# Kernel optimization log

Hardware: AMD Instinct MI355X
Metric: run time of the kernel (lower is better)

The kernel has to match this reference:

```python
import jax, jax.numpy as jnp
import numpy as np
from jax import lax

ANGRES = 5


def _conv(x, w, stride=(1, 1), pad=((1, 1), (1, 1)), dil=(1, 1)):
    return lax.conv_general_dilated(x, w, stride, pad, rhs_dilation=dil,
                                    dimension_numbers=('NCHW', 'OIHW', 'NCHW'))


def _lrelu(x):
    return jnp.where(x >= 0, x, 0.1 * x)


def _block_s(x, w):
    # SAI input: split into 5x5 grid of (sh,sw) views, conv each view, emit MacPI-interleaved layout
    B, C, H, W = x.shape
    sh, sw = H // 5, W // 5
    p = x.reshape(B, C, 5, sh, 5, sw).transpose(0, 2, 4, 1, 3, 5).reshape(B * 25, C, sh, sw)
    y = _conv(p, w).reshape(B, 5, 5, C, sh, sw)
    # (B,bi,bj,C,sh,sw) -> (B,C,sh,bi,sw,bj) -> (B,C,H,W)   [torch permute(0,3,4,1,5,2)]
    return y.transpose(0, 3, 4, 1, 5, 2).reshape(B, C, H, W)


def _block_a(x, w):
    # MacPI input: conv each 5x5 macropixel independently (zero pad at block edges)
    B, C, H, W = x.shape
    nh, nw = H // 5, W // 5
    p = x.reshape(B, C, nh, 5, nw, 5).transpose(0, 2, 4, 1, 3, 5).reshape(B * nh * nw, C, 5, 5)
    y = _conv(p, w)
    return y.reshape(B, nh, nw, C, 5, 5).transpose(0, 3, 1, 4, 2, 5).reshape(B, C, H, W)


def _epi(x, w1, w2, a):
    # EPI conv: [1,3a] kernel, stride [1,a], pad [0,a]; then 1x1 to a*C; then 1D pixel shuffle on W
    y = _lrelu(_conv(x, w1, stride=(1, a), pad=((0, 0), (a, a))))
    y = _lrelu(_conv(y, w2, pad=((0, 0), (0, 0))))
    B, aC, H, Wa = y.shape
    C = aC // a
    return y.reshape(B, a, C, H, Wa).transpose(0, 2, 3, 4, 1).reshape(B, C, H, Wa * a)


def _att_fuse(buf, alpha, gamma, beta, eps=1e-5):
    # covariance-based GLU attention over the N=4 branches
    B, NC, H, W = buf.shape
    N = 4
    C = NC // N
    x5 = buf.reshape(B, N, C, H, W)
    xr = x5.reshape(B, N, C * H * W)
    M = xr.shape[-1]
    xc = xr - jnp.mean(xr, axis=-1, keepdims=True)
    cov = jnp.einsum('bnm,bkm->bnk', xc, xc) * (alpha / (M - 1))  # [B,N,N]
    norm = cov / jnp.sqrt(jnp.mean(cov * cov, axis=(1, 2), keepdims=True) + eps)
    g = gamma * norm + beta
    att = g * jax.nn.sigmoid(g)  # GLU of duplicated halves
    out = jnp.einsum('bnk,bkm->bnm', att, xr).reshape(B, N, C, H, W) + x5
    return out.reshape(B, NC, H, W)


def _mac2sai(x, a):
    B, C, HU, WV = x.shape
    h, w = HU // a, WV // a
    return x.reshape(B, C, a, h, a, w).transpose(0, 1, 3, 5, 2, 4).reshape(B, C, h * a, w * a)


def _tsfefb(x, x1, ws, wa, we1, we2, al, ga, be, wf1, wf2, a):
    feaSpa = _lrelu(_block_s(x1, ws))
    feaAng = _lrelu(_block_a(x, wa))
    feaH = _epi(x, we1, we2, a)
    feaV = jnp.transpose(_epi(jnp.transpose(x, (0, 1, 3, 2)), we1, we2, a), (0, 1, 3, 2))
    buf = jnp.concatenate([feaSpa, feaAng, feaH, feaV], axis=1)
    out = _att_fuse(buf, al, ga, be)
    y = _lrelu(_conv(out, wf1, pad=((0, 0), (0, 0))))
    y = _conv(y, wf2, pad=((a, a), (a, a)), dil=(a, a))
    return y + x


def setup_inputs() -> dict:
    key = jax.random.key(0)
    ks = jax.random.split(key, 12)
    B, C, a, n = 4, 64, ANGRES, 4
    H = W = a * 32  # 160

    def w(k, shape):
        fan_in = float(np.prod(shape[2:]))
        return jax.random.normal(k, shape, jnp.float32) / np.float32(np.sqrt(fan_in))

    return {
        'x': jax.random.normal(ks[0], (B, C, H, W), jnp.float32),
        'x1': jax.random.normal(ks[1], (B, C, H, W), jnp.float32),
        'w_spa': w(ks[2], (n, C, C, 3, 3)),
        'w_ang': w(ks[3], (n, C, C, 3, 3)),
        'w_epi1': w(ks[4], (n, C, C, 1, 3 * a)),
        'w_epi2': w(ks[5], (n, a * C, C, 1, 1)),
        'alpha': jnp.ones((n,), jnp.float32),
        'gamma': 0.1 * jax.random.normal(ks[6], (n,), jnp.float32),
        'beta': 0.1 * jax.random.normal(ks[7], (n,), jnp.float32),
        'w_fuse1': w(ks[8], (n, C, 4 * C, 1, 1)),
        'w_fuse2': w(ks[9], (n, C, C, 3, 3)),
    }


def reference(x, x1, w_spa, w_ang, w_epi1, w_epi2, alpha, gamma, beta, w_fuse1, w_fuse2):
    a = ANGRES
    buf, buf1 = x, x1
    for i in range(w_spa.shape[0]):
        buf = _tsfefb(buf, buf1, w_spa[i], w_ang[i], w_epi1[i], w_epi2[i],
                      alpha[i], gamma[i], beta[i], w_fuse1[i], w_fuse2[i], a)
        buf1 = _mac2sai(buf, a)
    return buf
```

## Files before the change

### kernel.cpp

```cpp
#include <hip/hip_runtime.h>

__device__ __forceinline__ float lrelu(float v){ return v >= 0.f ? v : 0.1f*v; }


__global__ __launch_bounds__(256) void k_wrep(const float* __restrict__ wspa, const float* __restrict__ wang,
                                              const float* __restrict__ wf2, float* __restrict__ outp){
  int id = blockIdx.x*256 + threadIdx.x;
  int t = id / 147456, r = id - t*147456;
  int i = r / 36864,  e = r - i*36864;
  int ci = e / 576,   r3 = e - ci*576;
  int co = r3 / 9,    j = r3 - co*9;
  const float* src = (t==0 ? wspa : (t==1 ? wang : wf2));
  outp[id] = src[(size_t)i*36864 + co*576 + ci*9 + j];
}

__global__ __launch_bounds__(256) void k_spa(const float* __restrict__ buf1, const float* __restrict__ w,
                                             float* __restrict__ out){
  const int P = blockIdx.x;
  const int within = P >> 3, cog = within & 7, tsel = within >> 3;
  const int tg = (P & 7)*25 + tsel;
  const int b = tg / 50, r2 = tg % 50;
  const int view = r2 >> 1, half = r2 & 1;
  const int bi = view / 5, bj = view % 5;
  const int th0 = half*16;
  const int tid = threadIdx.x;
  __shared__ float plane[2][18*38];
  for (int idx=tid; idx<2*18*38; idx+=256) ((float*)plane)[idx]=0.f;
  float acc[2][8];
  #pragma unroll
  for (int k=0;k<2;k++)
    #pragma unroll
    for (int c=0;c<8;c++) acc[k][c]=0.f;
  const float* src = buf1 + (size_t)b*1638400 + bi*32*160 + bj*32;
  const int sr = tid >> 3, sq = (tid & 7)*4;
  const int vr = th0 - 1 + sr;
  const bool rowok = (tid < 144) && ((unsigned)vr < 32u);
  __syncthreads();
  if (rowok)
    *(float4*)&plane[0][sr*38 + 4 + sq] = *(const float4*)(src + vr*160 + sq);
  __syncthreads();
  const int lr2 = tid >> 5, c = tid & 31;
  for (int ci=0; ci<64; ci++){
    float4 nx;
    const bool ld = rowok && (ci < 63);
    if (ld) nx = *(const float4*)(src + (size_t)(ci+1)*25600 + vr*160 + sq);
    const float* P2 = plane[ci & 1];
    float g[4][3];
    {
      const float* pp = &P2[(2*lr2)*38 + c + 3];
      g[0][0]=pp[0];   g[0][1]=pp[1];   g[0][2]=pp[2];
      g[1][0]=pp[38];  g[1][1]=pp[39];  g[1][2]=pp[40];
      g[2][0]=pp[76];  g[2][1]=pp[77];  g[2][2]=pp[78];
      g[3][0]=pp[114]; g[3][1]=pp[115]; g[3][2]=pp[116];
    }
    const float* wrow = w + ci*576 + cog*72;
    #pragma unroll
    for (int co=0;co<8;co++){
      const float* wp = wrow + co*9;
      float w0=wp[0],w1=wp[1],w2=wp[2],w3=wp[3],w4=wp[4],w5=wp[5],w6=wp[6],w7=wp[7],w8=wp[8];
      acc[0][co] += g[0][0]*w0+g[0][1]*w1+g[0][2]*w2+g[1][0]*w3+g[1][1]*w4
                  + g[1][2]*w5+g[2][0]*w6+g[2][1]*w7+g[2][2]*w8;
      acc[1][co] += g[1][0]*w0+g[1][1]*w1+g[1][2]*w2+g[2][0]*w3+g[2][1]*w4
                  + g[2][2]*w5+g[3][0]*w6+g[3][1]*w7+g[3][2]*w8;
    }
    if (ld) *(float4*)&plane[(ci+1)&1][sr*38 + 4 + sq] = nx;
    __syncthreads();
  }
  #pragma unroll
  for (int k=0;k<2;k++){
    int si = th0 + 2*lr2 + k;
    int h = si*5 + bi, wq = c*5 + bj;
    #pragma unroll
    for (int co=0;co<8;co++){
      int ch = b*64 + cog*8 + co;
      out[(size_t)ch*25600 + h*160 + wq] = lrelu(acc[k][co]);
    }
  }
}

__global__ __launch_bounds__(320) void k_ang(const float* __restrict__ bufA, const float* __restrict__ w,
                                             float* __restrict__ out){
  const int P = blockIdx.x;
  const int within = P >> 3, cog = within & 15, tsel = within >> 4;
  const int tg = (P & 7)*8 + tsel;
  const int b = tg >> 4, mip = tg & 15;
  const int tid = threadIdx.x;
  __shared__ float lds[2][2296];
  for (int i=tid; i<2*2296; i+=320) ((float*)lds)[i] = 0.f;

  const int u = tid >> 6, mi_l = (tid >> 5) & 1, mp = tid & 31;
  int ro[3];
  #pragma unroll
  for (int du=0; du<3; du++)
    ro[du] = mi_l*1148 + (u+du)*164 + mp*5;
  const bool st1 = tid < 80;
  const int rr0 = tid/40,       q0 = tid%40;
  const int rr1 = (tid+320)/40, q1 = (tid+320)%40;
  const int dst0 = (rr0/5)*1148 + (1 + rr0%5)*164 + q0*4;
  const int dst1 = (rr1/5)*1148 + (1 + rr1%5)*164 + q1*4;
  const float* src = bufA + (size_t)b*1638400 + (size_t)(mip*10)*160;

  float acc[4][5];
  #pragma unroll
  for (int co=0;co<4;co++)
    #pragma unroll
    for (int v=0;v<5;v++) acc[co][v]=0.f;

  __syncthreads();
  {
    *(float4*)&lds[0][dst0] = *(const float4*)(src + rr0*160 + q0*4);
    if (st1)
      *(float4*)&lds[0][dst1] = *(const float4*)(src + rr1*160 + q1*4);
  }
  __syncthreads();
  for (int ci=0; ci<64; ci++){
    float4 n0, n1;
    if (ci < 63){
      n0 = *(const float4*)(src + (size_t)(ci+1)*25600 + rr0*160 + q0*4);
      if (st1) n1 = *(const float4*)(src + (size_t)(ci+1)*25600 + rr1*160 + q1*4);
    }
    const float* Pb = lds[ci & 1];
    float c[3][5];
    #pragma unroll
    for (int du=0;du<3;du++){
      const float* rp = &Pb[ro[du]];
      c[du][0]=rp[0]; c[du][1]=rp[1]; c[du][2]=rp[2]; c[du][3]=rp[3]; c[du][4]=rp[4];
    }
    const float* wrow = w + ci*576 + cog*36;
    #pragma unroll
    for (int co=0;co<4;co++){
      const float* wp = wrow + co*9;
      float w0=wp[0],w1=wp[1],w2=wp[2],w3=wp[3],w4=wp[4],w5=wp[5],w6=wp[6],w7=wp[7],w8=wp[8];
      acc[co][0] += c[0][0]*w1 + c[0][1]*w2
                  + c[1][0]*w4 + c[1][1]*w5
                  + c[2][0]*w7 + c[2][1]*w8;
      acc[co][1] += c[0][0]*w0 + c[0][1]*w1 + c[0][2]*w2
                  + c[1][0]*w3 + c[1][1]*w4 + c[1][2]*w5
                  + c[2][0]*w6 + c[2][1]*w7 + c[2][2]*w8;
      acc[co][2] += c[0][1]*w0 + c[0][2]*w1 + c[0][3]*w2
                  + c[1][1]*w3 + c[1][2]*w4 + c[1][3]*w5
                  + c[2][1]*w6 + c[2][2]*w7 + c[2][3]*w8;
      acc[co][3] += c[0][2]*w0 + c[0][3]*w1 + c[0][4]*w2
                  + c[1][2]*w3 + c[1][3]*w4 + c[1][4]*w5
                  + c[2][2]*w6 + c[2][3]*w7 + c[2][4]*w8;
      acc[co][4] += c[0][3]*w0 + c[0][4]*w1
                  + c[1][3]*w3 + c[1][4]*w4
                  + c[2][3]*w6 + c[2][4]*w7;
    }
    if (ci < 63){
      float* Q = lds[(ci+1)&1];
      *(float4*)&Q[dst0] = n0;
      if (st1) *(float4*)&Q[dst1] = n1;
    }
    __syncthreads();
  }
  const int h = (mip*2 + mi_l)*5 + u;
  const int wc0 = mp*5;
  #pragma unroll
  for (int co=0;co<4;co++){
    int ch = b*64 + cog*4 + co;
    float* op = out + (size_t)ch*25600 + (size_t)h*160 + wc0;
    op[0]=lrelu(acc[co][0]); op[1]=lrelu(acc[co][1]); op[2]=lrelu(acc[co][2]);
    op[3]=lrelu(acc[co][3]); op[4]=lrelu(acc[co][4]);
  }
}

__global__ __launch_bounds__(320) void k_epi(const float* __restrict__ bufA, const float* __restrict__ we1,
                                             const float* __restrict__ we2, float* __restrict__ out){
  const int bb = blockIdx.x >> 1, half = blockIdx.x & 1;
  const int b = bb / 160, hw = bb % 160;
  const int tid = threadIdx.x;
  __shared__ float rowp[64*96];
  __shared__ float y1s[64*16];
  const int lofs = half ? 0 : 8;
  const int xofs = half ? 72 : 0;
  for (int ft=tid; ft<1408; ft+=320){
    int ci = ft/22, q = ft - ci*22;
    *(float4*)&rowp[ci*96 + lofs + q*4] =
      *(const float4*)(bufA + (size_t)b*1638400 + (size_t)ci*25600 + (size_t)hw*160 + xofs + q*4);
  }
  for (int idx=tid; idx<512; idx+=320){
    int ci = idx>>3, j = idx&7;
    rowp[ci*96 + (half ? 88+j : j)] = 0.f;
  }
  __syncthreads();
  if (tid < 256){
    const int co = tid >> 2, wvl0 = (tid & 3)*4;
    const int a0 = 2 + wvl0*5;
    float acc[4];
    #pragma unroll
    for (int j=0;j<4;j++) acc[j]=0.f;
    const float* wp0 = we1 + (size_t)co*960;
    for (int ci=0; ci<64; ci++){
      float fl[32];
      const float* rp = &rowp[ci*96 + a0];
      #pragma unroll
      for (int m=0;m<16;m++) *(float2*)&fl[2*m] = *(const float2*)&rp[2*m];
      const float* wp = wp0 + ci*15;
      #pragma unroll
      for (int t=0;t<15;t++){
        float wt = wp[t];
        #pragma unroll
        for (int j=0;j<4;j++) acc[j] += fl[1 + j*5 + t]*wt;
      }
    }
    #pragma unroll
    for (int j=0;j<4;j++) y1s[co*16 + wvl0 + j] = lrelu(acc[j]);
  }
  __syncthreads();
  {
    const int oc = tid, kk = oc >> 6, c = oc & 63;
    float a2[16];
    #pragma unroll
    for (int wv=0;wv<16;wv++) a2[wv]=0.f;
    const float* wp = we2 + (size_t)oc*64;
    for (int ci=0; ci<64; ci++){
      float wt = wp[ci];
      const float* yp = &y1s[ci*16];
      #pragma unroll
      for (int wv=0; wv<16; wv++) a2[wv] += yp[wv]*wt;
    }
    float* y2s = rowp;
    #pragma unroll
    for (int wv=0; wv<16; wv++) y2s[c*84 + wv*5 + kk] = lrelu(a2[wv]);
  }
  __syncthreads();
  {
    const float* y2s = rowp;
    for (int k=0;k<4;k++){
      int f = (tid + k*320)*4;
      int c = f/80, rr = f - c*80;
      *(float4*)(out + (size_t)(b*64+c)*25600 + (size_t)hw*160 + half*80 + rr)
        = *(const float4*)&y2s[c*84+rr];
    }
  }
}

__global__ __launch_bounds__(256) void k_permV(const float* __restrict__ tmp, float* __restrict__ dst){
  const int bc = blockIdx.x;
  const int ti = blockIdx.y / 5, tj = blockIdx.y % 5;
  const int hw0 = ti*32, r0 = tj*32;
  const int lx = threadIdx.x & 31, ly = threadIdx.x >> 5;
  __shared__ float tile[32][33];
  const float* in = tmp + (size_t)bc*25600;
  float* outp = dst + (size_t)bc*25600;
  for (int yy=ly; yy<32; yy+=8)
    tile[yy][lx] = in[(size_t)(hw0+yy)*160 + r0 + lx];
  __syncthreads();
  for (int yy=ly; yy<32; yy+=8)
    outp[(size_t)(r0+yy)*160 + hw0 + lx] = tile[lx][yy];
}

__global__ __launch_bounds__(256) void k_permM(const float* __restrict__ A, float* __restrict__ dst){
  const int bc = blockIdx.x >> 5, hh = blockIdx.x & 31;
  const int tid = threadIdx.x;
  __shared__ float rows[5*160];
  const float* in = A + (size_t)bc*25600;
  if (tid < 200){
    int ai = tid/40, q = (tid - ai*40)*4;
    *(float4*)&rows[ai*160 + q] = *(const float4*)(in + (size_t)(ai*32+hh)*160 + q);
  }
  __syncthreads();
  float* outp = dst + (size_t)bc*25600 + (size_t)hh*800;
  for (int t=tid; t<800; t+=256){
    int ww = t/25, r2 = t - ww*25, ai = r2/5, aj = r2 - ai*5;
    outp[t] = rows[ai*160 + aj*32 + ww];
  }
}

__global__ __launch_bounds__(256) void k_red(const float* __restrict__ b0, const float* __restrict__ b1,
                                             const float* __restrict__ b2, const float* __restrict__ b3,
                                             float* __restrict__ part){
  const int b = blockIdx.y, blk = blockIdx.x;
  const int tid = threadIdx.x;
  const size_t off = (size_t)b*1638400 + (size_t)blk*25600;
  float s0=0,s1=0,s2=0,s3=0;
  float p00=0,p01=0,p02=0,p03=0,p11=0,p12=0,p13=0,p22=0,p23=0,p33=0;
  for (int it=0; it<25; it++){
    size_t m = off + it*1024 + tid*4;
    float4 x0 = *(const float4*)(b0+m);
    float4 x1 = *(const float4*)(b1+m);
    float4 x2 = *(const float4*)(b2+m);
    float4 x3 = *(const float4*)(b3+m);
    s0 += (x0.x+x0.y)+(x0.z+x0.w);
    s1 += (x1.x+x1.y)+(x1.z+x1.w);
    s2 += (x2.x+x2.y)+(x2.z+x2.w);
    s3 += (x3.x+x3.y)+(x3.z+x3.w);
    p00 += x0.x*x0.x+x0.y*x0.y+x0.z*x0.z+x0.w*x0.w;
    p01 += x0.x*x1.x+x0.y*x1.y+x0.z*x1.z+x0.w*x1.w;
    p02 += x0.x*x2.x+x0.y*x2.y+x0.z*x2.z+x0.w*x2.w;
    p03 += x0.x*x3.x+x0.y*x3.y+x0.z*x3.z+x0.w*x3.w;
    p11 += x1.x*x1.x+x1.y*x1.y+x1.z*x1.z+x1.w*x1.w;
    p12 += x1.x*x2.x+x1.y*x2.y+x1.z*x2.z+x1.w*x2.w;
    p13 += x1.x*x3.x+x1.y*x3.y+x1.z*x3.z+x1.w*x3.w;
    p22 += x2.x*x2.x+x2.y*x2.y+x2.z*x2.z+x2.w*x2.w;
    p23 += x2.x*x3.x+x2.y*x3.y+x2.z*x3.z+x2.w*x3.w;
    p33 += x3.x*x3.x+x3.y*x3.y+x3.z*x3.z+x3.w*x3.w;
  }
  float vals[14] = {s0,s1,s2,s3,p00,p01,p02,p03,p11,p12,p13,p22,p23,p33};
  __shared__ float red[4][14];
  int lane = tid & 63, wv = tid >> 6;
  #pragma unroll
  for (int j=0;j<14;j++){
    float v = vals[j];
    #pragma unroll
    for (int o=32;o>0;o>>=1) v += __shfl_down(v,o,64);
    if (lane==0) red[wv][j]=v;
  }
  __syncthreads();
  if (tid<14) part[((size_t)b*64+blk)*16 + tid] = red[0][tid]+red[1][tid]+red[2][tid]+red[3][tid];
}

__global__ __launch_bounds__(256) void k_attW(const float* __restrict__ part,
        const float* __restrict__ alpha, const float* __restrict__ gamma, const float* __restrict__ beta,
        int iblk, const float* __restrict__ wf1, float* __restrict__ Weff){
  const int b = blockIdx.x, tid = threadIdx.x;
  __shared__ float st[14];
  __shared__ float att[16];
  if (tid<14){
    float t=0;
    for (int blk=0;blk<64;blk++) t += part[((size_t)b*64+blk)*16 + tid];
    st[tid]=t;
  }
  __syncthreads();
  if (tid==0){
    const float M = 1638400.f;
    float s[4] = {st[0],st[1],st[2],st[3]};
    float S[4][4];
    S[0][0]=st[4];  S[0][1]=S[1][0]=st[5];  S[0][2]=S[2][0]=st[6];  S[0][3]=S[3][0]=st[7];
    S[1][1]=st[8];  S[1][2]=S[2][1]=st[9];  S[1][3]=S[3][1]=st[10];
    S[2][2]=st[11]; S[2][3]=S[3][2]=st[12]; S[3][3]=st[13];
    float al=alpha[iblk], ga=gamma[iblk], be=beta[iblk];
    float scale = al/(M-1.f);
    float cov[4][4], ss=0.f;
    for (int n=0;n<4;n++) for (int k=0;k<4;k++){
      float c = (S[n][k] - s[n]*s[k]/M)*scale;
      cov[n][k]=c; ss += c*c;
    }
    float rms = sqrtf(ss/16.f + 1e-5f);
    for (int n=0;n<4;n++) for (int k=0;k<4;k++){
      float g = ga*cov[n][k]/rms + be;
      att[n*4+k] = g/(1.f+expf(-g));
    }
  }
  __syncthreads();
  for (int idx=tid; idx<16384; idx+=256){
    int co=idx>>8, kc=idx&255, k=kc>>6, c=kc&63;
    float v = wf1[co*256+kc];
    #pragma unroll
    for (int n=0;n<4;n++) v += att[n*4+k]*wf1[co*256+n*64+c];
    Weff[(size_t)b*16384+idx] = v;
  }
}

__global__ __launch_bounds__(256) void k_fuse1(const float* b0, const float* __restrict__ b1,
                                               const float* __restrict__ b2, const float* __restrict__ b3,
                                               const float* __restrict__ Weff, float* y64){
  const int tile = blockIdx.x, b = blockIdx.y;
  const int px0 = tile*64;
  const int tid = threadIdx.x;
  const int ti = tid >> 4, tj = tid & 15;
  __shared__ float xs[64][68];
  __shared__ float wt[64][68];
  float acc[4][4];
  #pragma unroll
  for (int i=0;i<4;i++)
    #pragma unroll
    for (int j=0;j<4;j++) acc[i][j]=0.f;
  const float* bptr[4] = {b0,b1,b2,b3};
  for (int kb=0; kb<4; kb++){
    const float* xbk = bptr[kb] + (size_t)b*1638400 + px0;
    const float* wb = Weff + (size_t)b*16384 + kb*64;
    __syncthreads();
    for (int idx=tid; idx<4096; idx+=256){
      int kc=idx>>6, px=idx&63;
      xs[kc][px] = xbk[(size_t)kc*25600 + px];
    }
    for (int idx=tid; idx<4096; idx+=256){
      int co=idx>>6, k2=idx&63;
      wt[k2][co] = wb[co*256 + k2];
    }
    __syncthreads();
    for (int k2=0;k2<64;k2++){
      float4 a = *(const float4*)&wt[k2][ti*4];
      float4 v = *(const float4*)&xs[k2][tj*4];
      acc[0][0]+=a.x*v.x; acc[0][1]+=a.x*v.y; acc[0][2]+=a.x*v.z; acc[0][3]+=a.x*v.w;
      acc[1][0]+=a.y*v.x; acc[1][1]+=a.y*v.y; acc[1][2]+=a.y*v.z; acc[1][3]+=a.y*v.w;
      acc[2][0]+=a.z*v.x; acc[2][1]+=a.z*v.y; acc[2][2]+=a.z*v.z; acc[2][3]+=a.z*v.w;
      acc[3][0]+=a.w*v.x; acc[3][1]+=a.w*v.y; acc[3][2]+=a.w*v.z; acc[3][3]+=a.w*v.w;
    }
  }
  #pragma unroll
  for (int i=0;i<4;i++){
    int co = ti*4 + i;
    float4 o = make_float4(lrelu(acc[i][0]), lrelu(acc[i][1]), lrelu(acc[i][2]), lrelu(acc[i][3]));
    *(float4*)(y64 + ((size_t)(b*64+co))*25600 + px0 + tj*4) = o;
  }
}

template<int FINAL>
__global__ __launch_bounds__(256) void k_fuse2(const float* __restrict__ y64, const float* resid,
                                               const float* __restrict__ w, float* outp){
  const int P = blockIdx.x;
  const int within = P >> 3, cog = within & 7, tsel = within >> 3;
  const int tg = (P & 7)*25 + tsel;
  const int b = tg / 50, tile = tg % 50;
  const int th0 = (tile/5)*16, tw0 = (tile%5)*32;
  const int tid = threadIdx.x;
  __shared__ float plane[2][26*48];
  float acc[2][8];
  #pragma unroll
  for (int k=0;k<2;k++)
    #pragma unroll
    for (int c=0;c<8;c++) acc[k][c]=0.f;
  const float* src = y64 + (size_t)b*1638400;
  const int s0r = tid/12,        s0c = tid - (tid/12)*12;
  const int s1i = tid + 256;
  const int s1r = s1i/12,        s1c = s1i - (s1i/12)*12;
  const bool has1 = tid < 56;
  const int g0h = th0 - 5 + s0r, g0w = tw0 - 8 + s0c*4;
  const int g1h = th0 - 5 + s1r, g1w = tw0 - 8 + s1c*4;
  const bool v0 = ((unsigned)g0h < 160u) && ((unsigned)g0w < 160u);
  const bool v1 = has1 && ((unsigned)g1h < 160u) && ((unsigned)g1w < 160u);
  const int go0 = g0h*160 + g0w, go1 = g1h*160 + g1w;
  const int d0 = s0r*48 + s0c*4, d1 = s1r*48 + s1c*4;
  const float4 z4 = make_float4(0.f,0.f,0.f,0.f);
  {
    float4 x0 = v0 ? *(const float4*)(src + go0) : z4;
    *(float4*)&plane[0][d0] = x0;
    if (has1){
      float4 x1 = v1 ? *(const float4*)(src + go1) : z4;
      *(float4*)&plane[0][d1] = x1;
    }
  }
  __syncthreads();
  const int lr = tid >> 5, c = tid & 31;
  const int tap = lr*48 + c + 3;
  for (int ci=0; ci<64; ci++){
    float4 n0, n1;
    if (ci < 63){
      const float* sN = src + (size_t)(ci+1)*25600;
      n0 = v0 ? *(const float4*)(sN + go0) : z4;
      if (has1) n1 = v1 ? *(const float4*)(sN + go1) : z4;
    }
    const float* Pb = plane[ci & 1];
    float t0[9], t1[9];
    {
      const float* pp = &Pb[tap];
      t0[0]=pp[0];      t0[1]=pp[5];      t0[2]=pp[10];
      t0[3]=pp[240];    t0[4]=pp[245];    t0[5]=pp[250];
      t0[6]=pp[480];    t0[7]=pp[485];    t0[8]=pp[490];
      const float* qq = pp + 8*48;
      t1[0]=qq[0];      t1[1]=qq[5];      t1[2]=qq[10];
      t1[3]=qq[240];    t1[4]=qq[245];    t1[5]=qq[250];
      t1[6]=qq[480];    t1[7]=qq[485];    t1[8]=qq[490];
    }
    const float* wrow = w + ci*576 + cog*72;
    #pragma unroll
    for (int co=0;co<8;co++){
      const float* wp = wrow + co*9;
      float w0=wp[0],w1=wp[1],w2=wp[2],w3=wp[3],w4=wp[4],w5=wp[5],w6=wp[6],w7=wp[7],w8=wp[8];
      acc[0][co] += t0[0]*w0+t0[1]*w1+t0[2]*w2+t0[3]*w3+t0[4]*w4
                  + t0[5]*w5+t0[6]*w6+t0[7]*w7+t0[8]*w8;
      acc[1][co] += t1[0]*w0+t1[1]*w1+t1[2]*w2+t1[3]*w3+t1[4]*w4
                  + t1[5]*w5+t1[6]*w6+t1[7]*w7+t1[8]*w8;
    }
    if (ci < 63){
      float* Q = plane[(ci+1)&1];
      *(float4*)&Q[d0] = n0;
      if (has1) *(float4*)&Q[d1] = n1;
    }
    __syncthreads();
  }
  #pragma unroll
  for (int k=0;k<2;k++){
    int h = th0 + lr + k*8, wq = tw0 + c;
    #pragma unroll
    for (int co=0;co<8;co++){
      int cg = cog*8 + co;
      size_t base = ((size_t)(b*64+cg)*160 + h)*160 + wq;
      outp[base] = acc[k][co] + resid[base];
    }
  }
}

extern "C" void kernel_launch(void* const* d_in, const int* in_sizes, int n_in,
                              void* d_out, int out_size, void* d_ws, size_t ws_size,
                              hipStream_t stream){
  const float* x    = (const float*)d_in[0];
  const float* x1   = (const float*)d_in[1];
  const float* wspa = (const float*)d_in[2];
  const float* wang = (const float*)d_in[3];
  const float* we1  = (const float*)d_in[4];
  const float* we2  = (const float*)d_in[5];
  const float* al   = (const float*)d_in[6];
  const float* ga   = (const float*)d_in[7];
  const float* be   = (const float*)d_in[8];
  const float* wf1  = (const float*)d_in[9];
  const float* wf2  = (const float*)d_in[10];

  char* ws = (char*)d_ws;
  const size_t SLOT = 26214400;
  float* A  = (float*)(ws);
  float* Bv = (float*)(ws +   SLOT);
  float* T1 = (float*)(ws + 2*SLOT);
  float* T2 = (float*)(ws + 3*SLOT);
  float* part = (float*)(ws + 4*SLOT);
  float* Weff = (float*)(ws + 4*SLOT + 16384);
  float* Wrep = (float*)(ws + 4*SLOT + 16384 + 262144);
  float* WspaR = Wrep;
  float* WangR = Wrep + 147456;
  float* Wf2R  = Wrep + 2*147456;
  float* D = (float*)d_out;

  k_wrep<<<1728,256,0,stream>>>(wspa, wang, wf2, Wrep);

  for (int i=0;i<4;i++){
    const float* Asrc  = (i==0) ? x  : (const float*)A;
    const float* B1src = (i==0) ? x1 : (const float*)Bv;
    k_permV<<<dim3(256,25),256,0,stream>>>(Asrc, D);
    k_epi<<<1280,320,0,stream>>>(D, we1 + (size_t)i*61440, we2 + (size_t)i*20480, T2);
    k_spa<<<1600,256,0,stream>>>(B1src, WspaR + (size_t)i*36864, T1);
    k_permV<<<dim3(256,25),256,0,stream>>>(T2, Bv);
    k_ang<<<1024,320,0,stream>>>(Asrc, WangR + (size_t)i*36864, T2);
    k_epi<<<1280,320,0,stream>>>(Asrc, we1 + (size_t)i*61440, we2 + (size_t)i*20480, D);
    k_red<<<dim3(64,4),256,0,stream>>>(T1, T2, D, Bv, part);
    k_attW<<<4,256,0,stream>>>(part, al, ga, be, i, wf1 + (size_t)i*16384, Weff);
    k_fuse1<<<dim3(400,4),256,0,stream>>>(T1, T2, D, Bv, Weff, T1);
    if (i<3){
      k_fuse2<0><<<1600,256,0,stream>>>(T1, Asrc, Wf2R + (size_t)i*36864, A);
      k_permM<<<8192,256,0,stream>>>(A, Bv);
    } else {
      k_fuse2<1><<<1600,256,0,stream>>>(T1, Asrc, Wf2R + (size_t)i*36864, D);
    }
  }
}
```

Measured before the change: 2.807 ms.

## Give each wavefront a private LDS halo tile to drop block-wide barriers in spa and fuse2 convs

In the spatial 3x3 conv and the fuse2 dilated conv, each 64-lane wavefront now stages its own haloed input rows in a private double-buffered LDS region instead of sharing one block-wide plane. This removes the __syncthreads at every input-channel step and relies on wavefront-lockstep execution for LDS visibility. The cost is redundant halo loads across wavefronts (more global and LDS traffic) and a larger shared footprint. Correctness depends on implicit wave-level ordering, with no explicit wave barrier.

```diff
diff --git a/kernel.cpp b/kernel.cpp
--- a/kernel.cpp
+++ b/kernel.cpp
@@ -24,34 +24,34 @@
   const int bi = view / 5, bj = view % 5;
   const int th0 = half*16;
   const int tid = threadIdx.x;
-  __shared__ float plane[2][18*38];
-  for (int idx=tid; idx<2*18*38; idx+=256) ((float*)plane)[idx]=0.f;
+  const int wv = tid >> 6, lane = tid & 63;
+  __shared__ float wl[4][2][240];
+  for (int i=lane; i<480; i+=64) ((float*)wl[wv])[i] = 0.f;
   float acc[2][8];
   #pragma unroll
   for (int k=0;k<2;k++)
     #pragma unroll
-    for (int c=0;c<8;c++) acc[k][c]=0.f;
+    for (int c2=0;c2<8;c2++) acc[k][c2]=0.f;
   const float* src = buf1 + (size_t)b*1638400 + bi*32*160 + bj*32;
-  const int sr = tid >> 3, sq = (tid & 7)*4;
-  const int vr = th0 - 1 + sr;
-  const bool rowok = (tid < 144) && ((unsigned)vr < 32u);
-  __syncthreads();
+  const int srow = lane >> 3, sq = (lane & 7)*4;
+  const int vr = th0 + 4*wv - 1 + srow;
+  const bool rowok = (lane < 48) && ((unsigned)vr < 32u);
+  const int dst = srow*40 + 4 + sq;
   if (rowok)
-    *(float4*)&plane[0][sr*38 + 4 + sq] = *(const float4*)(src + vr*160 + sq);
-  __syncthreads();
-  const int lr2 = tid >> 5, c = tid & 31;
+    *(float4*)&wl[wv][0][dst] = *(const float4*)(src + vr*160 + sq);
+  const int lrl = (tid >> 5) & 1, c = tid & 31;
   for (int ci=0; ci<64; ci++){
     float4 nx;
     const bool ld = rowok && (ci < 63);
     if (ld) nx = *(const float4*)(src + (size_t)(ci+1)*25600 + vr*160 + sq);
-    const float* P2 = plane[ci & 1];
+    const float* Pb = wl[wv][ci & 1];
     float g[4][3];
     {
-      const float* pp = &P2[(2*lr2)*38 + c + 3];
+      const float* pp = &Pb[(2*lrl)*40 + c + 3];
       g[0][0]=pp[0];   g[0][1]=pp[1];   g[0][2]=pp[2];
-      g[1][0]=pp[38];  g[1][1]=pp[39];  g[1][2]=pp[40];
-      g[2][0]=pp[76];  g[2][1]=pp[77];  g[2][2]=pp[78];
-      g[3][0]=pp[114]; g[3][1]=pp[115]; g[3][2]=pp[116];
+      g[1][0]=pp[40];  g[1][1]=pp[41];  g[1][2]=pp[42];
+      g[2][0]=pp[80];  g[2][1]=pp[81];  g[2][2]=pp[82];
+      g[3][0]=pp[120]; g[3][1]=pp[121]; g[3][2]=pp[122];
     }
     const float* wrow = w + ci*576 + cog*72;
     #pragma unroll
@@ -63,12 +63,11 @@
       acc[1][co] += g[1][0]*w0+g[1][1]*w1+g[1][2]*w2+g[2][0]*w3+g[2][1]*w4
                   + g[2][2]*w5+g[3][0]*w6+g[3][1]*w7+g[3][2]*w8;
     }
-    if (ld) *(float4*)&plane[(ci+1)&1][sr*38 + 4 + sq] = nx;
-    __syncthreads();
+    if (ld) *(float4*)&wl[wv][(ci+1)&1][dst] = nx;
   }
   #pragma unroll
   for (int k=0;k<2;k++){
-    int si = th0 + 2*lr2 + k;
+    int si = th0 + 4*wv + 2*lrl + k;
     int h = si*5 + bi, wq = c*5 + bj;
     #pragma unroll
     for (int co=0;co<8;co++){
@@ -212,17 +211,17 @@
     const int oc = tid, kk = oc >> 6, c = oc & 63;
     float a2[16];
     #pragma unroll
-    for (int wv=0;wv<16;wv++) a2[wv]=0.f;
+    for (int wv2=0;wv2<16;wv2++) a2[wv2]=0.f;
     const float* wp = we2 + (size_t)oc*64;
     for (int ci=0; ci<64; ci++){
       float wt = wp[ci];
       const float* yp = &y1s[ci*16];
       #pragma unroll
-      for (int wv=0; wv<16; wv++) a2[wv] += yp[wv]*wt;
+      for (int wv2=0; wv2<16; wv2++) a2[wv2] += yp[wv2]*wt;
     }
     float* y2s = rowp;
     #pragma unroll
-    for (int wv=0; wv<16; wv++) y2s[c*84 + wv*5 + kk] = lrelu(a2[wv]);
+    for (int wv2=0; wv2<16; wv2++) y2s[c*84 + wv2*5 + kk] = lrelu(a2[wv2]);
   }
   __syncthreads();
   {
@@ -407,53 +406,52 @@
   const int b = tg / 50, tile = tg % 50;
   const int th0 = (tile/5)*16, tw0 = (tile%5)*32;
   const int tid = threadIdx.x;
-  __shared__ float plane[2][26*48];
+  const int wv = tid >> 6, lane = tid & 63;
+  __shared__ float wl[4][2][576];
+  for (int i=lane; i<1152; i+=64) ((float*)wl[wv])[i] = 0.f;
   float acc[2][8];
   #pragma unroll
   for (int k=0;k<2;k++)
     #pragma unroll
-    for (int c=0;c<8;c++) acc[k][c]=0.f;
+    for (int c2=0;c2<8;c2++) acc[k][c2]=0.f;
   const float* src = y64 + (size_t)b*1638400;
-  const int s0r = tid/12,        s0c = tid - (tid/12)*12;
-  const int s1i = tid + 256;
-  const int s1r = s1i/12,        s1c = s1i - (s1i/12)*12;
-  const bool has1 = tid < 56;
-  const int g0h = th0 - 5 + s0r, g0w = tw0 - 8 + s0c*4;
-  const int g1h = th0 - 5 + s1r, g1w = tw0 - 8 + s1c*4;
-  const bool v0 = ((unsigned)g0h < 160u) && ((unsigned)g0w < 160u);
-  const bool v1 = has1 && ((unsigned)g1h < 160u) && ((unsigned)g1w < 160u);
-  const int go0 = g0h*160 + g0w, go1 = g1h*160 + g1w;
-  const int d0 = s0r*48 + s0c*4, d1 = s1r*48 + s1c*4;
-  const float4 z4 = make_float4(0.f,0.f,0.f,0.f);
-  {
-    float4 x0 = v0 ? *(const float4*)(src + go0) : z4;
-    *(float4*)&plane[0][d0] = x0;
-    if (has1){
-      float4 x1 = v1 ? *(const float4*)(src + go1) : z4;
-      *(float4*)&plane[0][d1] = x1;
-    }
-  }
-  __syncthreads();
-  const int lr = tid >> 5, c = tid & 31;
-  const int tap = lr*48 + c + 3;
+  int sdst[3], soff[3];
+  bool sok[3];
+  #pragma unroll
+  for (int j=0;j<3;j++){
+    int m = lane + j*64;
+    bool act = m < 144;
+    int mm = act ? m : 0;
+    int srow = mm/12, q = mm - srow*12;
+    int dlt = srow + 3*(srow>=2) + (srow>=4) + (srow>=8) + 3*(srow>=10);
+    int gh = th0 - 5 + 2*wv + dlt, gw = tw0 - 8 + q*4;
+    sok[j] = act && ((unsigned)gh < 160u) && ((unsigned)gw < 160u);
+    soff[j] = gh*160 + gw;
+    sdst[j] = srow*48 + q*4;
+  }
+  #pragma unroll
+  for (int j=0;j<3;j++)
+    if (sok[j]) *(float4*)&wl[wv][0][sdst[j]] = *(const float4*)(src + soff[j]);
+  const int lrl = (tid >> 5) & 1, c = tid & 31;
+  const int t0base = lrl*48 + c + 3;
   for (int ci=0; ci<64; ci++){
-    float4 n0, n1;
+    float4 n0, n1, n2;
     if (ci < 63){
       const float* sN = src + (size_t)(ci+1)*25600;
-      n0 = v0 ? *(const float4*)(sN + go0) : z4;
-      if (has1) n1 = v1 ? *(const float4*)(sN + go1) : z4;
-    }
-    const float* Pb = plane[ci & 1];
+      if (sok[0]) n0 = *(const float4*)(sN + soff[0]);
+      if (sok[1]) n1 = *(const float4*)(sN + soff[1]);
+      if (sok[2]) n2 = *(const float4*)(sN + soff[2]);
+    }
+    const float* Pb = wl[wv][ci & 1];
     float t0[9], t1[9];
     {
-      const float* pp = &Pb[tap];
-      t0[0]=pp[0];      t0[1]=pp[5];      t0[2]=pp[10];
-      t0[3]=pp[240];    t0[4]=pp[245];    t0[5]=pp[250];
-      t0[6]=pp[480];    t0[7]=pp[485];    t0[8]=pp[490];
-      const float* qq = pp + 8*48;
-      t1[0]=qq[0];      t1[1]=qq[5];      t1[2]=qq[10];
-      t1[3]=qq[240];    t1[4]=qq[245];    t1[5]=qq[250];
-      t1[6]=qq[480];    t1[7]=qq[485];    t1[8]=qq[490];
+      const float* pp = &Pb[t0base];
+      t0[0]=pp[0];        t0[1]=pp[5];        t0[2]=pp[10];
+      t0[3]=pp[2*48];     t0[4]=pp[2*48+5];   t0[5]=pp[2*48+10];
+      t0[6]=pp[6*48];     t0[7]=pp[6*48+5];   t0[8]=pp[6*48+10];
+      t1[0]=pp[4*48];     t1[1]=pp[4*48+5];   t1[2]=pp[4*48+10];
+      t1[3]=pp[8*48];     t1[4]=pp[8*48+5];   t1[5]=pp[8*48+10];
+      t1[6]=pp[10*48];    t1[7]=pp[10*48+5];  t1[8]=pp[10*48+10];
     }
     const float* wrow = w + ci*576 + cog*72;
     #pragma unroll
@@ -466,15 +464,15 @@
                   + t1[5]*w5+t1[6]*w6+t1[7]*w7+t1[8]*w8;
     }
     if (ci < 63){
-      float* Q = plane[(ci+1)&1];
-      *(float4*)&Q[d0] = n0;
-      if (has1) *(float4*)&Q[d1] = n1;
-    }
-    __syncthreads();
+      float* Q = wl[wv][(ci+1)&1];
+      if (sok[0]) *(float4*)&Q[sdst[0]] = n0;
+      if (sok[1]) *(float4*)&Q[sdst[1]] = n1;
+      if (sok[2]) *(float4*)&Q[sdst[2]] = n2;
+    }
   }
   #pragma unroll
   for (int k=0;k<2;k++){
-    int h = th0 + lr + k*8, wq = tw0 + c;
+    int h = th0 + 2*wv + lrl + k*8, wq = tw0 + c;
     #pragma unroll
     for (int co=0;co<8;co++){
       int cg = cog*8 + co;
```

New measurement: 2.741 ms. 2.4% less time.
